# Kernel tuning notes

Measured on AMD Instinct MI355X. Metric: run time of the kernel, lower is better.

The kernel has to match this reference:

```python
import jax, jax.numpy as jnp
import numpy as np

N, D, H, E, K = 8192, 1024, 4096, 8, 2


def setup_inputs() -> dict:
    key = jax.random.key(0)
    ks = jax.random.split(key, 4)
    scaled = lambda k, shp, fan: (jax.random.normal(k, shp, jnp.float32) / np.sqrt(fan).astype(np.float32))
    return {
        "x": jax.random.normal(ks[0], (N, D), jnp.float32),
        "Wg": scaled(ks[1], (D, E), D),
        "bg": jnp.zeros((E,), jnp.float32),
        "W1": scaled(ks[2], (E, D, H), D),
        "b1": jnp.zeros((E, H), jnp.float32),
        "W2": scaled(ks[3], (E, H, D), H),
        "b2": jnp.zeros((E, D), jnp.float32),
    }


def reference(x, Wg, bg, W1, b1, W2, b2):
    # Gating: softmax over experts, top-k selection, renormalize top-k probs.
    gate_probs = jax.nn.softmax(x @ Wg + bg, axis=-1)            # [N, E]
    topk_p, topk_i = jax.lax.top_k(gate_probs, K)                # [N, K]
    topk_p = topk_p / topk_p.sum(axis=-1, keepdims=True)
    onehot = jax.nn.one_hot(topk_i, E, dtype=x.dtype)            # [N, K, E]
    # Per-token combine weight for each expert (0 if expert not in top-k).
    w = (onehot * topk_p[..., None]).sum(axis=1)                 # [N, E]

    out = jnp.zeros_like(x)
    for e in range(E):  # fixed small loop over structurally distinct experts
        h = jax.nn.relu(x @ W1[e] + b1[e])                       # dropout = identity (eval)
        out = out + w[:, e:e + 1] * (h @ W2[e] + b2[e])

    # Load-balancing auxiliary loss.
    importance = gate_probs.sum(axis=0)
    importance = importance / importance.sum()
    load = onehot.sum(axis=(0, 1)) / (x.shape[0] * K)            # [E]
    lb_loss = E * (importance * load).sum()
    return out, lb_loss
```

## Files before the change

kernel.cpp:

```cpp
#include <hip/hip_runtime.h>
#include <hip/hip_bf16.h>
#include <math.h>

#define NTOK 8192
#define DDIM 1024
#define HDIM 4096
#define NEXP 8
#define KTOP 2
#define MAXROWS 16896
#define MAXTILES 264

typedef __bf16 bf16x8 __attribute__((ext_vector_type(8)));
typedef float f32x4 __attribute__((ext_vector_type(4)));

#define GAS __attribute__((address_space(1)))
#define LAS __attribute__((address_space(3)))

__device__ __forceinline__ void async16(const void* g, void* l) {
  __builtin_amdgcn_global_load_lds((GAS void*)g, (LAS void*)l, 16, 0, 0);
}

#define XB_OFF     ((size_t)0)
#define W1T_OFF    (XB_OFF + (size_t)NTOK*DDIM*2)
#define ROWOUT_OFF W1T_OFF
#define W2T_OFF    (W1T_OFF + (size_t)NEXP*DDIM*HDIM*2)
#define HB_OFF     (W2T_OFF + (size_t)NEXP*HDIM*DDIM*2)
#define ROWTOK_OFF (HB_OFF + (size_t)MAXROWS*HDIM*2)
#define ROWW_OFF   (ROWTOK_OFF + (size_t)MAXROWS*4)
#define TOKE_OFF   (ROWW_OFF + (size_t)MAXROWS*4)
#define TOKW_OFF   (TOKE_OFF + (size_t)NTOK*KTOP*4)
#define TOKROW_OFF (TOKW_OFF + (size_t)NTOK*KTOP*4)
#define TILEE_OFF  (TOKROW_OFF + (size_t)NTOK*KTOP*4)
#define CNT_OFF    (TILEE_OFF + (size_t)512*4)
#define POS_OFF    (CNT_OFF + 64)
#define IMP_OFF    (POS_OFF + 64)
#define META_OFF   (IMP_OFF + 64)

__global__ void init_kernel(int* counts, float* importance) {
  if (threadIdx.x < NEXP) { counts[threadIdx.x] = 0; importance[threadIdx.x] = 0.f; }
}

__global__ void cast_x_kernel(const float* __restrict__ src, __hip_bfloat16* __restrict__ dst) {
  size_t i = ((size_t)blockIdx.x * blockDim.x + threadIdx.x) * 4;
  if (i < (size_t)NTOK * DDIM) {
    float4 v = *(const float4*)(src + i);
    dst[i + 0] = __float2bfloat16(v.x);
    dst[i + 1] = __float2bfloat16(v.y);
    dst[i + 2] = __float2bfloat16(v.z);
    dst[i + 3] = __float2bfloat16(v.w);
  }
}

__global__ __launch_bounds__(256) void transpose_cast_kernel(
    const float* __restrict__ src, __hip_bfloat16* __restrict__ dst, int R, int C) {
  __shared__ float tile[64][65];
  const int e = blockIdx.z;
  const float* s = src + (size_t)e * R * C;
  __hip_bfloat16* d = dst + (size_t)e * R * C;
  const int c0 = blockIdx.x * 64, r0 = blockIdx.y * 64;
  const int tc = (threadIdx.x & 15) * 4;
  const int tr = threadIdx.x >> 4;
#pragma unroll
  for (int p = 0; p < 4; ++p) {
    float4 v = *(const float4*)&s[(size_t)(r0 + tr + p * 16) * C + c0 + tc];
    tile[tr + p * 16][tc + 0] = v.x;
    tile[tr + p * 16][tc + 1] = v.y;
    tile[tr + p * 16][tc + 2] = v.z;
    tile[tr + p * 16][tc + 3] = v.w;
  }
  __syncthreads();
  const int oc = threadIdx.x >> 4;
  const int orr = (threadIdx.x & 15) * 4;
#pragma unroll
  for (int p = 0; p < 4; ++p) {
    const int c = oc + p * 16;
    __hip_bfloat16 tmp[4];
    tmp[0] = __float2bfloat16(tile[orr + 0][c]);
    tmp[1] = __float2bfloat16(tile[orr + 1][c]);
    tmp[2] = __float2bfloat16(tile[orr + 2][c]);
    tmp[3] = __float2bfloat16(tile[orr + 3][c]);
    *(ushort4*)&d[(size_t)(c0 + c) * R + r0 + orr] = *(ushort4*)tmp;
  }
}

__global__ __launch_bounds__(256) void gating_kernel(
    const float* __restrict__ x, const float* __restrict__ Wg, const float* __restrict__ bg,
    int* __restrict__ tok_e, float* __restrict__ tok_w,
    int* __restrict__ counts, float* __restrict__ importance) {
  const int tid = threadIdx.x, wid = tid >> 6, lane = tid & 63;
  const int t = blockIdx.x * 32 + wid * 8 + (lane >> 3);
  const int e = lane & 7;
  const float* xr = x + (size_t)t * DDIM;
  double dot = 0.0;
  for (int d = 0; d < DDIM; d += 4) {
    float4 xv = *(const float4*)(xr + d);
    dot += (double)xv.x * (double)Wg[(d + 0) * NEXP + e];
    dot += (double)xv.y * (double)Wg[(d + 1) * NEXP + e];
    dot += (double)xv.z * (double)Wg[(d + 2) * NEXP + e];
    dot += (double)xv.w * (double)Wg[(d + 3) * NEXP + e];
  }
  double logit = dot + (double)bg[e];
  double m = logit;
  for (int off = 1; off < 8; off <<= 1) {
    double o = __shfl_xor(m, off, 64);
    m = o > m ? o : m;
  }
  double p = exp(logit - m);
  double s = p;
  for (int off = 1; off < 8; off <<= 1) s += __shfl_xor(s, off, 64);
  float prob = (float)(p / s);

  __shared__ float imp[NEXP];
  __shared__ int cnt[NEXP];
  if (tid < NEXP) { imp[tid] = 0.f; cnt[tid] = 0; }
  __syncthreads();
  atomicAdd(&imp[e], prob);

  float bp = prob; int be = e;
  for (int off = 1; off < 8; off <<= 1) {
    float op = __shfl_xor(bp, off, 64); int oe = __shfl_xor(be, off, 64);
    if (op > bp || (op == bp && oe < be)) { bp = op; be = oe; }
  }
  float p2 = (e == be) ? -1.f : prob;
  float sp = p2; int se = e;
  for (int off = 1; off < 8; off <<= 1) {
    float op = __shfl_xor(sp, off, 64); int oe = __shfl_xor(se, off, 64);
    if (op > sp || (op == sp && oe < se)) { sp = op; se = oe; }
  }
  if (e == 0) {
    float tsum = bp + sp;
    tok_e[t * 2 + 0] = be; tok_e[t * 2 + 1] = se;
    tok_w[t * 2 + 0] = bp / tsum; tok_w[t * 2 + 1] = sp / tsum;
    atomicAdd(&cnt[be], 1); atomicAdd(&cnt[se], 1);
  }
  __syncthreads();
  if (tid < NEXP) {
    atomicAdd(&counts[tid], cnt[tid]);
    atomicAdd(&importance[tid], imp[tid]);
  }
}

__global__ void offsets_kernel(const int* __restrict__ counts, int* pos, int* tile_expert,
                               int* meta, int* row_token) {
  if (threadIdx.x == 0) {
    int pb = 0, tb = 0;
    for (int e = 0; e < NEXP; e++) {
      pos[e] = pb;
      int tiles = (counts[e] + 63) >> 6;
      for (int tt = 0; tt < tiles; ++tt) tile_expert[tb + tt] = e;
      pb += tiles * 64; tb += tiles;
    }
    meta[0] = tb;
  }
  __syncthreads();
  for (int i = threadIdx.x; i < MAXROWS; i += blockDim.x) row_token[i] = -1;
}

__global__ void scatter_kernel(const int* __restrict__ tok_e, const float* __restrict__ tok_w,
                               int* __restrict__ pos, int* __restrict__ row_token,
                               float* __restrict__ row_weight, int* __restrict__ tok_row) {
  __shared__ int lcnt[NEXP], lbase[NEXP];
  const int t = blockIdx.x * 256 + threadIdx.x;
  if (threadIdx.x < NEXP) lcnt[threadIdx.x] = 0;
  __syncthreads();
  const int e0 = tok_e[t * 2 + 0], e1 = tok_e[t * 2 + 1];
  const int s0 = atomicAdd(&lcnt[e0], 1);
  const int s1 = atomicAdd(&lcnt[e1], 1);
  __syncthreads();
  if (threadIdx.x < NEXP) lbase[threadIdx.x] = atomicAdd(&pos[threadIdx.x], lcnt[threadIdx.x]);
  __syncthreads();
  int r0 = lbase[e0] + s0; row_token[r0] = t; row_weight[r0] = tok_w[t * 2 + 0]; tok_row[t * 2 + 0] = r0;
  int r1 = lbase[e1] + s1; row_token[r1] = t; row_weight[r1] = tok_w[t * 2 + 1]; tok_row[t * 2 + 1] = r1;
}

template<int NDIM, int KDIM, bool GATHER, bool RELU>
__global__ __launch_bounds__(256) void moe_gemm_kernel(
    const __hip_bfloat16* __restrict__ Ag, const __hip_bfloat16* __restrict__ Bg,
    const float* __restrict__ bias, __hip_bfloat16* __restrict__ Cg,
    const int* __restrict__ row_token, const int* __restrict__ tile_expert,
    const int* __restrict__ meta) {
  const int NCOLT = NDIM / 256;
  const int ty = blockIdx.x / NCOLT;
  const int cx = blockIdx.x % NCOLT;
  if (ty >= meta[0]) return;
  const int e = tile_expert[ty];
  const int r0 = ty * 64;
  const int n0 = cx * 256;
  const int tid = threadIdx.x;
  const int wid = tid >> 6, lane = tid & 63;

  __shared__ __align__(16) __hip_bfloat16 As[2][64 * 32];
  __shared__ __align__(16) __hip_bfloat16 Bs[2][256 * 32];

  const int g = (((lane & 3) - ((lane >> 2) & 3) - (lane >> 4)) & 3) * 8;
  const int srl = lane >> 2;
  const __hip_bfloat16* ga;
  if (GATHER) {
    int t = row_token[r0 + wid * 16 + srl]; if (t < 0) t = 0;
    ga = Ag + (size_t)t * KDIM + g;
  } else {
    ga = Ag + (size_t)(r0 + wid * 16 + srl) * KDIM + g;
  }
  const __hip_bfloat16* gb[4];
#pragma unroll
  for (int c = 0; c < 4; ++c)
    gb[c] = Bg + ((size_t)e * NDIM + n0 + wid * 64 + c * 16 + srl) * KDIM + g;
  const int ldsA = wid * 16 * 32;
  const int ldsB = wid * 64 * 32;

  f32x4 acc[4][4] = {};
  const int wn = wid * 64;
  const int fr = lane & 15;
  const int soff = (((lane >> 4) + (lane & 3) + ((lane >> 2) & 3)) & 3) * 8;

#define STAGE(b) do { \
    async16(ga, &As[b][ldsA]); \
    async16(gb[0], &Bs[b][ldsB]); \
    async16(gb[1], &Bs[b][ldsB + 16 * 32]); \
    async16(gb[2], &Bs[b][ldsB + 32 * 32]); \
    async16(gb[3], &Bs[b][ldsB + 48 * 32]); \
    ga += 32; gb[0] += 32; gb[1] += 32; gb[2] += 32; gb[3] += 32; } while (0)

  STAGE(0);
  const int NT = KDIM / 32;
  for (int kt = 0; kt < NT; ++kt) {
    const int cur = kt & 1;
    __syncthreads();
    if (kt + 1 < NT) { if (cur) STAGE(0); else STAGE(1); }
    bf16x8 av[4], bv[4];
#pragma unroll
    for (int i = 0; i < 4; i++) av[i] = *(const bf16x8*)&As[cur][(i * 16 + fr) * 32 + soff];
#pragma unroll
    for (int j = 0; j < 4; j++) bv[j] = *(const bf16x8*)&Bs[cur][(wn + j * 16 + fr) * 32 + soff];
#pragma unroll
    for (int i = 0; i < 4; i++)
#pragma unroll
      for (int j = 0; j < 4; j++)
        acc[i][j] = __builtin_amdgcn_mfma_f32_16x16x32_bf16(av[i], bv[j], acc[i][j], 0, 0, 0);
  }
#undef STAGE

  const int crow = (lane >> 4) * 4;
  const int ccol = lane & 15;
#pragma unroll
  for (int j = 0; j < 4; j++) {
    const int gc = n0 + wn + j * 16 + ccol;
    const float bb = bias[e * NDIM + gc];
#pragma unroll
    for (int i = 0; i < 4; i++) {
      const int grb = r0 + i * 16 + crow;
#pragma unroll
      for (int r = 0; r < 4; r++) {
        float v = acc[i][j][r] + bb;
        if (RELU) v = v > 0.f ? v : 0.f;
        Cg[(size_t)(grb + r) * NDIM + gc] = __float2bfloat16(v);
      }
    }
  }
}

__global__ __launch_bounds__(256) void combine_kernel(
    const __hip_bfloat16* __restrict__ rowout, const int* __restrict__ tok_row,
    const float* __restrict__ row_weight, float* __restrict__ out) {
  const int idx = blockIdx.x * 256 + threadIdx.x;
  const int t = idx >> 7;
  const int d = (idx & 127) * 8;
  const int r0 = tok_row[t * 2 + 0], r1 = tok_row[t * 2 + 1];
  const float w0 = row_weight[r0], w1 = row_weight[r1];
  bf16x8 a = *(const bf16x8*)&rowout[(size_t)r0 * DDIM + d];
  bf16x8 b = *(const bf16x8*)&rowout[(size_t)r1 * DDIM + d];
  float o[8];
#pragma unroll
  for (int k = 0; k < 8; k++) o[k] = w0 * (float)a[k] + w1 * (float)b[k];
  float* dst = out + (size_t)t * DDIM + d;
  *(float4*)(dst + 0) = make_float4(o[0], o[1], o[2], o[3]);
  *(float4*)(dst + 4) = make_float4(o[4], o[5], o[6], o[7]);
}

__global__ void finalize_kernel(const float* __restrict__ importance,
                                const int* __restrict__ counts, float* __restrict__ lb_out) {
  if (threadIdx.x == 0 && blockIdx.x == 0) {
    float s = 0.f;
    for (int e = 0; e < NEXP; e++) s += importance[e];
    float lb = 0.f;
    for (int e = 0; e < NEXP; e++)
      lb += (importance[e] / s) * ((float)counts[e] / (float)(NTOK * KTOP));
    lb_out[0] = (float)NEXP * lb;
  }
}

extern "C" void kernel_launch(void* const* d_in, const int* in_sizes, int n_in,
                              void* d_out, int out_size, void* d_ws, size_t ws_size,
                              hipStream_t stream) {
  (void)in_sizes; (void)n_in; (void)out_size; (void)ws_size;
  const float* x  = (const float*)d_in[0];
  const float* Wg = (const float*)d_in[1];
  const float* bg = (const float*)d_in[2];
  const float* W1 = (const float*)d_in[3];
  const float* b1 = (const float*)d_in[4];
  const float* W2 = (const float*)d_in[5];
  const float* b2 = (const float*)d_in[6];
  float* out = (float*)d_out;

  char* ws = (char*)d_ws;
  __hip_bfloat16* xb     = (__hip_bfloat16*)(ws + XB_OFF);
  __hip_bfloat16* w1t    = (__hip_bfloat16*)(ws + W1T_OFF);
  __hip_bfloat16* rowout = (__hip_bfloat16*)(ws + ROWOUT_OFF);
  __hip_bfloat16* w2t    = (__hip_bfloat16*)(ws + W2T_OFF);
  __hip_bfloat16* hb     = (__hip_bfloat16*)(ws + HB_OFF);
  int*   row_token  = (int*)(ws + ROWTOK_OFF);
  float* row_weight = (float*)(ws + ROWW_OFF);
  int*   tok_e   = (int*)(ws + TOKE_OFF);
  float* tok_w   = (float*)(ws + TOKW_OFF);
  int*   tok_row = (int*)(ws + TOKROW_OFF);
  int*   tile_e  = (int*)(ws + TILEE_OFF);
  int*   counts  = (int*)(ws + CNT_OFF);
  int*   pos     = (int*)(ws + POS_OFF);
  float* importance = (float*)(ws + IMP_OFF);
  int*   meta    = (int*)(ws + META_OFF);

  init_kernel<<<1, 64, 0, stream>>>(counts, importance);
  cast_x_kernel<<<NTOK * DDIM / 4 / 256, 256, 0, stream>>>(x, xb);
  transpose_cast_kernel<<<dim3(HDIM / 64, DDIM / 64, NEXP), 256, 0, stream>>>(W1, w1t, DDIM, HDIM);
  transpose_cast_kernel<<<dim3(DDIM / 64, HDIM / 64, NEXP), 256, 0, stream>>>(W2, w2t, HDIM, DDIM);
  gating_kernel<<<NTOK / 32, 256, 0, stream>>>(x, Wg, bg, tok_e, tok_w, counts, importance);
  offsets_kernel<<<1, 256, 0, stream>>>(counts, pos, tile_e, meta, row_token);
  scatter_kernel<<<NTOK / 256, 256, 0, stream>>>(tok_e, tok_w, pos, row_token, row_weight, tok_row);
  moe_gemm_kernel<HDIM, DDIM, true, true>
      <<<MAXTILES * (HDIM / 256), 256, 0, stream>>>(xb, w1t, b1, hb, row_token, tile_e, meta);
  moe_gemm_kernel<DDIM, HDIM, false, false>
      <<<MAXTILES * (DDIM / 256), 256, 0, stream>>>(hb, w2t, b2, rowout, row_token, tile_e, meta);
  combine_kernel<<<NTOK * 128 / 256, 256, 0, stream>>>(rowout, tok_row, row_weight, out);
  finalize_kernel<<<1, 64, 0, stream>>>(importance, counts, out + (size_t)NTOK * DDIM);
}
```

Measured before the change: 840.5 us.

## Retile MoE GEMM to 256x128 blocks with larger per-wave output and XOR swizzle

```diff
diff --git a/kernel.cpp b/kernel.cpp
--- a/kernel.cpp
+++ b/kernel.cpp
@@ -7,8 +7,8 @@
 #define HDIM 4096
 #define NEXP 8
 #define KTOP 2
-#define MAXROWS 16896
-#define MAXTILES 264
+#define MAXROWS 18432
+#define MAXTILES 72
 
 typedef __bf16 bf16x8 __attribute__((ext_vector_type(8)));
 typedef float f32x4 __attribute__((ext_vector_type(4)));
@@ -31,7 +31,7 @@
 #define TOKW_OFF   (TOKE_OFF + (size_t)NTOK*KTOP*4)
 #define TOKROW_OFF (TOKW_OFF + (size_t)NTOK*KTOP*4)
 #define TILEE_OFF  (TOKROW_OFF + (size_t)NTOK*KTOP*4)
-#define CNT_OFF    (TILEE_OFF + (size_t)512*4)
+#define CNT_OFF    (TILEE_OFF + (size_t)256*4)
 #define POS_OFF    (CNT_OFF + 64)
 #define IMP_OFF    (POS_OFF + 64)
 #define META_OFF   (IMP_OFF + 64)
@@ -146,9 +146,9 @@
     int pb = 0, tb = 0;
     for (int e = 0; e < NEXP; e++) {
       pos[e] = pb;
-      int tiles = (counts[e] + 63) >> 6;
+      int tiles = (counts[e] + 255) >> 8;
       for (int tt = 0; tt < tiles; ++tt) tile_expert[tb + tt] = e;
-      pb += tiles * 64; tb += tiles;
+      pb += tiles * 256; tb += tiles;
     }
     meta[0] = tb;
   }
@@ -173,53 +173,52 @@
   int r1 = lbase[e1] + s1; row_token[r1] = t; row_weight[r1] = tok_w[t * 2 + 1]; tok_row[t * 2 + 1] = r1;
 }
 
-template<int NDIM, int KDIM, bool GATHER, bool RELU>
-__global__ __launch_bounds__(256) void moe_gemm_kernel(
+template<int NDIM, int KDIM, int NCOLT, bool GATHER, bool RELU>
+__global__ __launch_bounds__(256, 2) void moe_gemm_kernel(
     const __hip_bfloat16* __restrict__ Ag, const __hip_bfloat16* __restrict__ Bg,
     const float* __restrict__ bias, __hip_bfloat16* __restrict__ Cg,
     const int* __restrict__ row_token, const int* __restrict__ tile_expert,
     const int* __restrict__ meta) {
-  const int NCOLT = NDIM / 256;
   const int ty = blockIdx.x / NCOLT;
   const int cx = blockIdx.x % NCOLT;
   if (ty >= meta[0]) return;
   const int e = tile_expert[ty];
-  const int r0 = ty * 64;
-  const int n0 = cx * 256;
-  const int tid = threadIdx.x;
-  const int wid = tid >> 6, lane = tid & 63;
-
-  __shared__ __align__(16) __hip_bfloat16 As[2][64 * 32];
-  __shared__ __align__(16) __hip_bfloat16 Bs[2][256 * 32];
-
-  const int g = (((lane & 3) - ((lane >> 2) & 3) - (lane >> 4)) & 3) * 8;
-  const int srl = lane >> 2;
-  const __hip_bfloat16* ga;
-  if (GATHER) {
-    int t = row_token[r0 + wid * 16 + srl]; if (t < 0) t = 0;
-    ga = Ag + (size_t)t * KDIM + g;
-  } else {
-    ga = Ag + (size_t)(r0 + wid * 16 + srl) * KDIM + g;
-  }
-  const __hip_bfloat16* gb[4];
-#pragma unroll
-  for (int c = 0; c < 4; ++c)
-    gb[c] = Bg + ((size_t)e * NDIM + n0 + wid * 64 + c * 16 + srl) * KDIM + g;
-  const int ldsA = wid * 16 * 32;
-  const int ldsB = wid * 64 * 32;
-
-  f32x4 acc[4][4] = {};
-  const int wn = wid * 64;
+  const int r0 = ty * 256;
+  const int n0 = cx * 128;
+  const int tid = threadIdx.x, wid = tid >> 6, lane = tid & 63;
+
+  __shared__ __align__(16) __hip_bfloat16 As[2][256 * 32];
+  __shared__ __align__(16) __hip_bfloat16 Bs[2][128 * 32];
+
+  const int rl = lane >> 2;
+  const int g = ((lane & 3) ^ (rl & 3)) * 8;
+  const __hip_bfloat16* gA[4];
+  const __hip_bfloat16* gB[2];
+#pragma unroll
+  for (int m = 0; m < 4; ++m) {
+    const int row = wid * 64 + m * 16 + rl;
+    if (GATHER) {
+      int t = row_token[r0 + row]; if (t < 0) t = 0;
+      gA[m] = Ag + (size_t)t * KDIM + g;
+    } else {
+      gA[m] = Ag + (size_t)(r0 + row) * KDIM + g;
+    }
+  }
+#pragma unroll
+  for (int m = 0; m < 2; ++m)
+    gB[m] = Bg + ((size_t)e * NDIM + n0 + wid * 32 + m * 16 + rl) * KDIM + g;
+  const int ldsA = wid * 4 * 512;
+  const int ldsB = wid * 2 * 512;
+
+  f32x4 acc[4][8] = {};
   const int fr = lane & 15;
-  const int soff = (((lane >> 4) + (lane & 3) + ((lane >> 2) & 3)) & 3) * 8;
+  const int soff = ((lane >> 4) ^ (lane & 3)) * 8;
 
 #define STAGE(b) do { \
-    async16(ga, &As[b][ldsA]); \
-    async16(gb[0], &Bs[b][ldsB]); \
-    async16(gb[1], &Bs[b][ldsB + 16 * 32]); \
-    async16(gb[2], &Bs[b][ldsB + 32 * 32]); \
-    async16(gb[3], &Bs[b][ldsB + 48 * 32]); \
-    ga += 32; gb[0] += 32; gb[1] += 32; gb[2] += 32; gb[3] += 32; } while (0)
+    async16(gA[0], &As[b][ldsA]);        async16(gA[1], &As[b][ldsA + 512]); \
+    async16(gA[2], &As[b][ldsA + 1024]); async16(gA[3], &As[b][ldsA + 1536]); \
+    async16(gB[0], &Bs[b][ldsB]);        async16(gB[1], &Bs[b][ldsB + 512]); \
+    gA[0] += 32; gA[1] += 32; gA[2] += 32; gA[3] += 32; gB[0] += 32; gB[1] += 32; } while (0)
 
   STAGE(0);
   const int NT = KDIM / 32;
@@ -227,15 +226,17 @@
     const int cur = kt & 1;
     __syncthreads();
     if (kt + 1 < NT) { if (cur) STAGE(0); else STAGE(1); }
-    bf16x8 av[4], bv[4];
-#pragma unroll
-    for (int i = 0; i < 4; i++) av[i] = *(const bf16x8*)&As[cur][(i * 16 + fr) * 32 + soff];
-#pragma unroll
-    for (int j = 0; j < 4; j++) bv[j] = *(const bf16x8*)&Bs[cur][(wn + j * 16 + fr) * 32 + soff];
+    bf16x8 av[4], bv[8];
 #pragma unroll
     for (int i = 0; i < 4; i++)
-#pragma unroll
-      for (int j = 0; j < 4; j++)
+      av[i] = *(const bf16x8*)&As[cur][(wid * 64 + i * 16 + fr) * 32 + soff];
+#pragma unroll
+    for (int j = 0; j < 8; j++)
+      bv[j] = *(const bf16x8*)&Bs[cur][(j * 16 + fr) * 32 + soff];
+#pragma unroll
+    for (int i = 0; i < 4; i++)
+#pragma unroll
+      for (int j = 0; j < 8; j++)
         acc[i][j] = __builtin_amdgcn_mfma_f32_16x16x32_bf16(av[i], bv[j], acc[i][j], 0, 0, 0);
   }
 #undef STAGE
@@ -243,17 +244,17 @@
   const int crow = (lane >> 4) * 4;
   const int ccol = lane & 15;
 #pragma unroll
-  for (int j = 0; j < 4; j++) {
-    const int gc = n0 + wn + j * 16 + ccol;
+  for (int j = 0; j < 8; j++) {
+    const int gc = n0 + j * 16 + ccol;
     const float bb = bias[e * NDIM + gc];
 #pragma unroll
     for (int i = 0; i < 4; i++) {
-      const int grb = r0 + i * 16 + crow;
+      const int gr = r0 + wid * 64 + i * 16 + crow;
 #pragma unroll
       for (int r = 0; r < 4; r++) {
         float v = acc[i][j][r] + bb;
         if (RELU) v = v > 0.f ? v : 0.f;
-        Cg[(size_t)(grb + r) * NDIM + gc] = __float2bfloat16(v);
+        Cg[(size_t)(gr + r) * NDIM + gc] = __float2bfloat16(v);
       }
     }
   }
@@ -326,10 +327,10 @@
   gating_kernel<<<NTOK / 32, 256, 0, stream>>>(x, Wg, bg, tok_e, tok_w, counts, importance);
   offsets_kernel<<<1, 256, 0, stream>>>(counts, pos, tile_e, meta, row_token);
   scatter_kernel<<<NTOK / 256, 256, 0, stream>>>(tok_e, tok_w, pos, row_token, row_weight, tok_row);
-  moe_gemm_kernel<HDIM, DDIM, true, true>
-      <<<MAXTILES * (HDIM / 256), 256, 0, stream>>>(xb, w1t, b1, hb, row_token, tile_e, meta);
-  moe_gemm_kernel<DDIM, HDIM, false, false>
-      <<<MAXTILES * (DDIM / 256), 256, 0, stream>>>(hb, w2t, b2, rowout, row_token, tile_e, meta);
+  moe_gemm_kernel<HDIM, DDIM, HDIM / 128, true, true>
+      <<<MAXTILES * (HDIM / 128), 256, 0, stream>>>(xb, w1t, b1, hb, row_token, tile_e, meta);
+  moe_gemm_kernel<DDIM, HDIM, DDIM / 128, false, false>
+      <<<MAXTILES * (DDIM / 128), 256, 0, stream>>>(hb, w2t, b2, rowout, row_token, tile_e, meta);
   combine_kernel<<<NTOK * 128 / 256, 256, 0, stream>>>(rowout, tok_row, row_weight, out);
   finalize_kernel<<<1, 64, 0, stream>>>(importance, counts, out + (size_t)NTOK * DDIM);
 }
```

Measured after the change: 946.9 us. +12.7%, slower.
